# Performance work log

Measured on AMD Instinct MI355X. Metric: run time of the kernel, lower is better.

Reference implementation:

```python
import jax, jax.numpy as jnp
import numpy as np

D_KQ = 8  # per-head key/query dim, matches module constant

def setup_inputs() -> dict:
    key = jax.random.key(0)
    kx, kq, kk, kv = jax.random.split(key, 4)
    x = jax.random.normal(kx, (4, 1024, 4), dtype=jnp.float32)        # [B,S,d_in]
    # torch.rand -> uniform[0,1) init, stacked over heads: [H,d_in,d]
    Wq = jax.random.uniform(kq, (32, 4, 8), dtype=jnp.float32)
    Wk = jax.random.uniform(kk, (32, 4, 8), dtype=jnp.float32)
    Wv = jax.random.uniform(kv, (32, 4, 8), dtype=jnp.float32)
    return {"x": x, "Wq": Wq, "Wk": Wk, "Wv": Wv}

def reference(x, Wq, Wk, Wv):
    # Batched equivalent of the per-head Python loop.
    q = jnp.einsum('bsi,hik->bhsk', x, Wq)   # [B,H,S,d_kq]
    k = jnp.einsum('bsi,hik->bhsk', x, Wk)   # [B,H,S,d_kq]
    v = jnp.einsum('bsi,hiv->bhsv', x, Wv)   # [B,H,S,d_v]
    scores = jnp.einsum('bhsk,bhtk->bhst', q, k) / jnp.sqrt(jnp.float32(D_KQ))
    w = jax.nn.softmax(scores, axis=-1)      # [B,H,S,S]
    ctx = jnp.einsum('bhst,bhtv->bhsv', w, v)  # [B,H,S,d_v]
    B, H, S, dv = ctx.shape
    # torch.cat(head_outputs, dim=-1) == interleave heads last: [B,S,H*d_v]
    return ctx.transpose(0, 2, 1, 3).reshape(B, S, H * dv)
```

## Files before the change

### kernel.cpp

```cpp
#include <hip/hip_runtime.h>
#include <hip/hip_bf16.h>
#include <math.h>

#define SEQ  1024
#define NH   32

typedef __attribute__((ext_vector_type(8))) short short8_t;
typedef __attribute__((ext_vector_type(4))) short short4_t;
typedef __attribute__((ext_vector_type(4))) float float4_t;

__device__ inline float exp2_fast(float x) {
#if __has_builtin(__builtin_amdgcn_exp2f)
    return __builtin_amdgcn_exp2f(x);
#else
    return exp2f(x);
#endif
}

__device__ inline short f2bf(float f) {
    __hip_bfloat16 h = __float2bfloat16(f);
    return *reinterpret_cast<short*>(&h);
}

__global__ __launch_bounds__(512, 8) void mha_mfma_kernel(
    const float* __restrict__ x,
    const float* __restrict__ Wq,
    const float* __restrict__ Wk,
    const float* __restrict__ Wv,
    float* __restrict__ out)
{
    const int bid = blockIdx.x;
    const int rc  = bid & 7;
    const int h   = (bid >> 3) & 31;
    const int b   = bid >> 8;

    const int tid  = threadIdx.x;
    const int lane = tid & 63;
    const int wv   = tid >> 6;
    const int l15  = lane & 15;
    const int g    = lane >> 4;

    __shared__ short xbf[SEQ][4];
    __shared__ short xT[8][1032];

    const float4* xg = (const float4*)(x + (size_t)b * SEQ * 4);
    for (int i = tid; i < SEQ; i += 512) {
        float4 v = xg[i];
        short s0 = f2bf(v.x), s1 = f2bf(v.y), s2 = f2bf(v.z), s3 = f2bf(v.w);
        short4_t pk = {s0, s1, s2, s3};
        *(short4_t*)(&xbf[i][0]) = pk;
        xT[0][i] = s0; xT[1][i] = s1; xT[2][i] = s2; xT[3][i] = s3;
    }
    for (int i = tid; i < SEQ; i += 512) {
        xT[4][i] = (short)0x3F80;
        xT[5][i] = 0; xT[6][i] = 0; xT[7][i] = 0;
    }

    const int srow = rc * 128 + wv * 16 + l15;
    const float4 xs = xg[srow];
    const float* wqp = Wq + h * 32;
    const float* wkp = Wk + h * 32;
    float q[8];
#pragma unroll
    for (int m = 0; m < 8; ++m)
        q[m] = xs.x * wqp[m] + xs.y * wqp[8 + m] + xs.z * wqp[16 + m] + xs.w * wqp[24 + m];
    const float cs = 0.35355339059327373f * 1.4426950408889634f;
    short8_t yfrag = {0, 0, 0, 0, 0, 0, 0, 0};
    if (lane < 16) {
#pragma unroll
        for (int i = 0; i < 4; ++i) {
            float yv = 0.f;
#pragma unroll
            for (int m = 0; m < 8; ++m) yv += q[m] * wkp[i * 8 + m];
            yfrag[i] = f2bf(yv * cs);
        }
    }

    __syncthreads();

    const short* abase = (lane < 16) ? &xbf[8 * (l15 >> 2) + (l15 & 3)][0] : &xT[5][0];
    const int    astep = (lane < 16) ? 128 : 0;
    const short* vbase = &xT[l15 & 7][0] + 8 * g;

    float4_t zacc = {0.f, 0.f, 0.f, 0.f};
    const float4_t cz = {0.f, 0.f, 0.f, 0.f};

#pragma unroll 4
    for (int it = 0; it < 32; ++it) {
        short4_t a1lo = *(const short4_t*)abase;
        short4_t a2lo = *(const short4_t*)(abase + 16);
        short8_t a1 = {a1lo[0], a1lo[1], a1lo[2], a1lo[3], 0, 0, 0, 0};
        short8_t a2 = {a2lo[0], a2lo[1], a2lo[2], a2lo[3], 0, 0, 0, 0};

        float4_t c1 = __builtin_amdgcn_mfma_f32_16x16x32_bf16(a1, yfrag, cz, 0, 0, 0);
        float4_t c2 = __builtin_amdgcn_mfma_f32_16x16x32_bf16(a2, yfrag, cz, 0, 0, 0);

        short8_t wf;
        wf[0] = f2bf(exp2_fast(c1[0]));
        wf[1] = f2bf(exp2_fast(c1[1]));
        wf[2] = f2bf(exp2_fast(c1[2]));
        wf[3] = f2bf(exp2_fast(c1[3]));
        wf[4] = f2bf(exp2_fast(c2[0]));
        wf[5] = f2bf(exp2_fast(c2[1]));
        wf[6] = f2bf(exp2_fast(c2[2]));
        wf[7] = f2bf(exp2_fast(c2[3]));

        short8_t av = *(const short8_t*)vbase;
        zacc = __builtin_amdgcn_mfma_f32_16x16x32_bf16(av, wf, zacc, 0, 0, 0);

        abase += astep;
        vbase += 32;
    }

    float lsum = __shfl(zacc[0], 16 + l15);
    float z0 = __shfl(zacc[0], l15);
    float z1 = __shfl(zacc[1], l15);
    float z2 = __shfl(zacc[2], l15);
    float z3 = __shfl(zacc[3], l15);
    if (lane < 32) {
        const float inv = 1.f / lsum;
        const float* wvp = Wv + h * 32 + g * 4;
        float4 o;
        o.x = inv * (z0 * wvp[0] + z1 * wvp[8]  + z2 * wvp[16] + z3 * wvp[24]);
        o.y = inv * (z0 * wvp[1] + z1 * wvp[9]  + z2 * wvp[17] + z3 * wvp[25]);
        o.z = inv * (z0 * wvp[2] + z1 * wvp[10] + z2 * wvp[18] + z3 * wvp[26]);
        o.w = inv * (z0 * wvp[3] + z1 * wvp[11] + z2 * wvp[19] + z3 * wvp[27]);
        float4* op = (float4*)(out + (size_t)(b * SEQ + srow) * (NH * 8) + h * 8 + g * 4);
        *op = o;
    }
}

extern "C" void kernel_launch(void* const* d_in, const int* in_sizes, int n_in,
                              void* d_out, int out_size, void* d_ws, size_t ws_size,
                              hipStream_t stream) {
    const float* x  = (const float*)d_in[0];
    const float* Wq = (const float*)d_in[1];
    const float* Wk = (const float*)d_in[2];
    const float* Wv = (const float*)d_in[3];
    float* out = (float*)d_out;

    const int B = in_sizes[0] / (SEQ * 4);
    dim3 grid(B * NH * (SEQ / 128));
    dim3 block(512);
    hipLaunchKernelGGL(mha_mfma_kernel, grid, block, 0, stream, x, Wq, Wk, Wv, out);
}
```

Measured before the change: 25.56 us.

## Process two query row groups per wave to reuse key/value fragments

Each wave now handles 32 query rows (two 16-row groups) instead of 16. The A-operand key loads and V fragment loads are shared across both groups, and the grid and launch-bounds occupancy hint are halved to match. The aim is to amortize LDS reads and the per-block x staging over twice the work, and to put more independent MFMA chains in flight. The cost is more registers per thread and half as many blocks, which lowers parallelism on a large GPU. The output stage is restructured so all 64 lanes write results, with the upper two lane groups selecting the second row group.

```diff
diff --git a/kernel.cpp b/kernel.cpp
--- a/kernel.cpp
+++ b/kernel.cpp
@@ -22,7 +22,7 @@
     return *reinterpret_cast<short*>(&h);
 }
 
-__global__ __launch_bounds__(512, 8) void mha_mfma_kernel(
+__global__ __launch_bounds__(512, 4) void mha_mfma_kernel(
     const float* __restrict__ x,
     const float* __restrict__ Wq,
     const float* __restrict__ Wk,
@@ -30,9 +30,9 @@
     float* __restrict__ out)
 {
     const int bid = blockIdx.x;
-    const int rc  = bid & 7;
-    const int h   = (bid >> 3) & 31;
-    const int b   = bid >> 8;
+    const int rc  = bid & 3;
+    const int h   = (bid >> 2) & 31;
+    const int b   = bid >> 7;
 
     const int tid  = threadIdx.x;
     const int lane = tid & 63;
@@ -50,29 +50,32 @@
         short4_t pk = {s0, s1, s2, s3};
         *(short4_t*)(&xbf[i][0]) = pk;
         xT[0][i] = s0; xT[1][i] = s1; xT[2][i] = s2; xT[3][i] = s3;
-    }
-    for (int i = tid; i < SEQ; i += 512) {
         xT[4][i] = (short)0x3F80;
         xT[5][i] = 0; xT[6][i] = 0; xT[7][i] = 0;
     }
 
-    const int srow = rc * 128 + wv * 16 + l15;
-    const float4 xs = xg[srow];
+    const int rowA = rc * 256 + wv * 32 + l15;
+    const int rowB = rowA + 16;
     const float* wqp = Wq + h * 32;
     const float* wkp = Wk + h * 32;
-    float q[8];
-#pragma unroll
-    for (int m = 0; m < 8; ++m)
-        q[m] = xs.x * wqp[m] + xs.y * wqp[8 + m] + xs.z * wqp[16 + m] + xs.w * wqp[24 + m];
     const float cs = 0.35355339059327373f * 1.4426950408889634f;
-    short8_t yfrag = {0, 0, 0, 0, 0, 0, 0, 0};
+    short8_t yA = {0,0,0,0,0,0,0,0};
+    short8_t yB = {0,0,0,0,0,0,0,0};
     if (lane < 16) {
+        float4 xsA = xg[rowA];
+        float4 xsB = xg[rowB];
 #pragma unroll
         for (int i = 0; i < 4; ++i) {
-            float yv = 0.f;
+            float ya = 0.f, yb = 0.f;
 #pragma unroll
-            for (int m = 0; m < 8; ++m) yv += q[m] * wkp[i * 8 + m];
-            yfrag[i] = f2bf(yv * cs);
+            for (int m = 0; m < 8; ++m) {
+                float qa = xsA.x * wqp[m] + xsA.y * wqp[8 + m] + xsA.z * wqp[16 + m] + xsA.w * wqp[24 + m];
+                float qb = xsB.x * wqp[m] + xsB.y * wqp[8 + m] + xsB.z * wqp[16 + m] + xsB.w * wqp[24 + m];
+                ya += qa * wkp[i * 8 + m];
+                yb += qb * wkp[i * 8 + m];
+            }
+            yA[i] = f2bf(ya * cs);
+            yB[i] = f2bf(yb * cs);
         }
     }
 
@@ -82,7 +85,8 @@
     const int    astep = (lane < 16) ? 128 : 0;
     const short* vbase = &xT[l15 & 7][0] + 8 * g;
 
-    float4_t zacc = {0.f, 0.f, 0.f, 0.f};
+    float4_t zA = {0.f, 0.f, 0.f, 0.f};
+    float4_t zB = {0.f, 0.f, 0.f, 0.f};
     const float4_t cz = {0.f, 0.f, 0.f, 0.f};
 
 #pragma unroll 4
@@ -91,43 +95,58 @@
         short4_t a2lo = *(const short4_t*)(abase + 16);
         short8_t a1 = {a1lo[0], a1lo[1], a1lo[2], a1lo[3], 0, 0, 0, 0};
         short8_t a2 = {a2lo[0], a2lo[1], a2lo[2], a2lo[3], 0, 0, 0, 0};
+        short8_t av = *(const short8_t*)vbase;
 
-        float4_t c1 = __builtin_amdgcn_mfma_f32_16x16x32_bf16(a1, yfrag, cz, 0, 0, 0);
-        float4_t c2 = __builtin_amdgcn_mfma_f32_16x16x32_bf16(a2, yfrag, cz, 0, 0, 0);
+        float4_t c1A = __builtin_amdgcn_mfma_f32_16x16x32_bf16(a1, yA, cz, 0, 0, 0);
+        float4_t c2A = __builtin_amdgcn_mfma_f32_16x16x32_bf16(a2, yA, cz, 0, 0, 0);
+        float4_t c1B = __builtin_amdgcn_mfma_f32_16x16x32_bf16(a1, yB, cz, 0, 0, 0);
+        float4_t c2B = __builtin_amdgcn_mfma_f32_16x16x32_bf16(a2, yB, cz, 0, 0, 0);
 
-        short8_t wf;
-        wf[0] = f2bf(exp2_fast(c1[0]));
-        wf[1] = f2bf(exp2_fast(c1[1]));
-        wf[2] = f2bf(exp2_fast(c1[2]));
-        wf[3] = f2bf(exp2_fast(c1[3]));
-        wf[4] = f2bf(exp2_fast(c2[0]));
-        wf[5] = f2bf(exp2_fast(c2[1]));
-        wf[6] = f2bf(exp2_fast(c2[2]));
-        wf[7] = f2bf(exp2_fast(c2[3]));
+        short8_t wfA, wfB;
+#pragma unroll
+        for (int i = 0; i < 4; ++i) {
+            wfA[i]     = f2bf(exp2_fast(c1A[i]));
+            wfA[4 + i] = f2bf(exp2_fast(c2A[i]));
+            wfB[i]     = f2bf(exp2_fast(c1B[i]));
+            wfB[4 + i] = f2bf(exp2_fast(c2B[i]));
+        }
 
-        short8_t av = *(const short8_t*)vbase;
-        zacc = __builtin_amdgcn_mfma_f32_16x16x32_bf16(av, wf, zacc, 0, 0, 0);
+        zA = __builtin_amdgcn_mfma_f32_16x16x32_bf16(av, wfA, zA, 0, 0, 0);
+        zB = __builtin_amdgcn_mfma_f32_16x16x32_bf16(av, wfB, zB, 0, 0, 0);
 
         abase += astep;
         vbase += 32;
     }
 
-    float lsum = __shfl(zacc[0], 16 + l15);
-    float z0 = __shfl(zacc[0], l15);
-    float z1 = __shfl(zacc[1], l15);
-    float z2 = __shfl(zacc[2], l15);
-    float z3 = __shfl(zacc[3], l15);
-    if (lane < 32) {
-        const float inv = 1.f / lsum;
-        const float* wvp = Wv + h * 32 + g * 4;
-        float4 o;
-        o.x = inv * (z0 * wvp[0] + z1 * wvp[8]  + z2 * wvp[16] + z3 * wvp[24]);
-        o.y = inv * (z0 * wvp[1] + z1 * wvp[9]  + z2 * wvp[17] + z3 * wvp[25]);
-        o.z = inv * (z0 * wvp[2] + z1 * wvp[10] + z2 * wvp[18] + z3 * wvp[26]);
-        o.w = inv * (z0 * wvp[3] + z1 * wvp[11] + z2 * wvp[19] + z3 * wvp[27]);
-        float4* op = (float4*)(out + (size_t)(b * SEQ + srow) * (NH * 8) + h * 8 + g * 4);
-        *op = o;
-    }
+    float lsA = __shfl(zA[0], 16 + l15);
+    float a0  = __shfl(zA[0], l15);
+    float a1e = __shfl(zA[1], l15);
+    float a2e = __shfl(zA[2], l15);
+    float a3e = __shfl(zA[3], l15);
+    float lsB = __shfl(zB[0], 16 + l15);
+    float b0  = __shfl(zB[0], l15);
+    float b1e = __shfl(zB[1], l15);
+    float b2e = __shfl(zB[2], l15);
+    float b3e = __shfl(zB[3], l15);
+
+    const int  isB  = g >> 1;
+    const int  half = g & 1;
+    const float lsum = isB ? lsB : lsA;
+    const float z0 = isB ? b0 : a0;
+    const float z1 = isB ? b1e : a1e;
+    const float z2 = isB ? b2e : a2e;
+    const float z3 = isB ? b3e : a3e;
+    const int srow = rowA - l15 + (isB ? 16 : 0) + l15;
+
+    const float inv = 1.f / lsum;
+    const float* wvp = Wv + h * 32 + half * 4;
+    float4 o;
+    o.x = inv * (z0 * wvp[0] + z1 * wvp[8]  + z2 * wvp[16] + z3 * wvp[24]);
+    o.y = inv * (z0 * wvp[1] + z1 * wvp[9]  + z2 * wvp[17] + z3 * wvp[25]);
+    o.z = inv * (z0 * wvp[2] + z1 * wvp[10] + z2 * wvp[18] + z3 * wvp[26]);
+    o.w = inv * (z0 * wvp[3] + z1 * wvp[11] + z2 * wvp[19] + z3 * wvp[27]);
+    float4* op = (float4*)(out + (size_t)(b * SEQ + srow) * (NH * 8) + h * 8 + half * 4);
+    *op = o;
 }
 
 extern "C" void kernel_launch(void* const* d_in, const int* in_sizes, int n_in,
@@ -140,7 +159,7 @@
     float* out = (float*)d_out;
 
     const int B = in_sizes[0] / (SEQ * 4);
-    dim3 grid(B * NH * (SEQ / 128));
+    dim3 grid(B * NH * (SEQ / 256));
     dim3 block(512);
     hipLaunchKernelGGL(mha_mfma_kernel, grid, block, 0, stream, x, Wq, Wk, Wv, out);
 }
```

Result: faster. 24.22 us (-5.3%).
